# Performance work log

Hardware: AMD Instinct MI355X
Metric: run time of the kernel (lower is better)

Reference implementation:

```python
import jax, jax.numpy as jnp
import numpy as np

K = 512
D = 64


def setup_inputs() -> dict:
    key = jax.random.key(0)
    k1, k2 = jax.random.split(key)
    z_e_x = jax.random.normal(k1, (32, D, 64, 64), dtype=jnp.float32)  # [B, D, H, W]
    # codebook initialized uniform(-1/K, 1/K) as in the torch module
    emb = jax.random.uniform(k2, (K, D), dtype=jnp.float32, minval=-1.0 / K, maxval=1.0 / K)
    return {"z_e_x": z_e_x, "emb": emb}


def reference(z_e_x, emb):
    B, Dc, H, W = z_e_x.shape
    # [B, D, H, W] -> [B*H*W, D]
    z = jnp.transpose(z_e_x, (0, 2, 3, 1)).reshape(-1, Dc)
    z_norm = jnp.sum(z * z, axis=1, keepdims=True)          # [N, 1]
    e_norm = jnp.sum(emb * emb, axis=1)[None, :]            # [1, K]
    dists = z_norm + e_norm - 2.0 * (z @ emb.T)             # [N, K]
    dists = dists.reshape(B, H, W, -1)
    latents = jnp.argmin(dists, axis=-1)                    # [B, H, W] int
    return latents
```

## Files before the change

### kernel.cpp

```cpp
#include <hip/hip_runtime.h>

#define KCODES 512
#define DDIM   64
#define NROWS  131072

typedef short bf16x8 __attribute__((ext_vector_type(8)));
typedef float f32x4  __attribute__((ext_vector_type(4)));
typedef int   i32x4  __attribute__((ext_vector_type(4)));

union frag_cast { i32x4 i; bf16x8 h; };

__device__ __forceinline__ unsigned cvt_pk_bf16(float x0, float x1) {
    unsigned r;
    asm volatile("v_cvt_pk_bf16_f32 %0, %1, %2" : "=v"(r) : "v"(x0), "v"(x1));
    return r;
}

__device__ __forceinline__ void split_pair(float x0, float x1, unsigned& h, unsigned& l) {
    h = cvt_pk_bf16(x0, x1);
    float hf0 = __uint_as_float(h << 16);
    float hf1 = __uint_as_float(h & 0xffff0000u);
    l = cvt_pk_bf16(x0 - hf0, x1 - hf1);
}

__device__ __forceinline__ void gload16(const void* g, void* l) {
    __builtin_amdgcn_global_load_lds(
        (const __attribute__((address_space(1))) void*)g,
        (__attribute__((address_space(3))) void*)l, 16, 0, 0);
}

__global__ __launch_bounds__(64) void k1_prep(const float* __restrict__ emb,
                                              float* __restrict__ en, float* __restrict__ emaxp,
                                              i32x4* __restrict__ efP) {
    const int kt = blockIdx.x, t = threadIdx.x;
    const int krow = t & 15, gq = t >> 4;
    const int k = kt * 16 + krow;

    float er[16];
    float pz = 0.f;
#pragma unroll
    for (int c = 0; c < 2; ++c)
#pragma unroll
        for (int j = 0; j < 8; ++j) {
            float x = emb[k * DDIM + c * 32 + gq * 8 + j];
            er[c * 8 + j] = x;
            pz = fmaf(x, x, pz);
        }

#pragma unroll
    for (int c = 0; c < 2; ++c) {
        i32x4 wh, wl;
#pragma unroll
        for (int i = 0; i < 4; ++i) {
            unsigned h, l;
            split_pair(er[c * 8 + 2 * i], er[c * 8 + 2 * i + 1], h, l);
            wh[i] = (int)h;
            wl[i] = (int)l;
        }
        efP[kt * 256 + c * 64 + krow + 16 * gq]       = wh;
        efP[kt * 256 + (2 + c) * 64 + krow + 16 * gq] = wl;
    }

    pz += __shfl_xor(pz, 16);
    pz += __shfl_xor(pz, 32);
    if (t < 16) en[k] = pz;

    float m = pz;
#pragma unroll
    for (int sh = 1; sh <= 8; sh <<= 1) m = fmaxf(m, __shfl_xor(m, sh));
    if (t == 0) emaxp[kt] = m;
}

__global__ __launch_bounds__(256, 4) void k3_fused(
    const float* __restrict__ z, const float* __restrict__ emb,
    const i32x4* __restrict__ efP,
    const float* __restrict__ en_g, const float* __restrict__ emaxp,
    int* __restrict__ out) {

    __shared__ i32x4 sfrag[2][8][4][64];
    __shared__ float en_l[KCODES];
    __shared__ float zn_l[128];
    __shared__ float zrow_s[4][64];
    __shared__ int   flag_rows[128];
    __shared__ int   nflag;

    const int t = threadIdx.x, blk = blockIdx.x;
    const int n0 = blk * 128;
    const int b = n0 >> 12, hw0 = n0 & 4095;
    const int w = t >> 6, lane = t & 63;
    const int klane = lane & 15, g = lane >> 4;

    if (t == 0) nflag = 0;

    auto issue_chunk = [&](int kg, int bsel) {
        const i32x4* src = efP + (size_t)kg * 2048;
        i32x4* dst = &sfrag[bsel][0][0][0];
#pragma unroll
        for (int i = 0; i < 8; ++i) {
            int q = w * 8 + i;
            gload16(src + q * 64 + lane, dst + q * 64);
        }
    };
    issue_chunk(0, 0);

    en_l[t] = en_g[t];
    en_l[t + 256] = en_g[t + 256];

    float em2 = 0.f;
#pragma unroll
    for (int i = 0; i < 32; ++i) em2 = fmaxf(em2, emaxp[i]);
    const float emax = sqrtf(em2) * 1.0001f;

    const float* zbase = z + (size_t)b * (DDIM * 4096) + hw0;
    bf16x8 zh[2][2], zl[2][2];
#pragma unroll
    for (int tl = 0; tl < 2; ++tl) {
        const int row = w * 32 + tl * 16 + klane;
        float zv[16];
#pragma unroll
        for (int c = 0; c < 2; ++c)
#pragma unroll
            for (int j = 0; j < 8; ++j)
                zv[c * 8 + j] = zbase[(size_t)(c * 32 + g * 8 + j) * 4096 + row];
        float pz = 0.f;
#pragma unroll
        for (int c = 0; c < 2; ++c) {
            frag_cast uh, ul;
#pragma unroll
            for (int i = 0; i < 4; ++i) {
                float x0 = zv[c * 8 + 2 * i], x1 = zv[c * 8 + 2 * i + 1];
                pz = fmaf(x0, x0, pz);
                pz = fmaf(x1, x1, pz);
                unsigned h, l;
                split_pair(x0, x1, h, l);
                uh.i[i] = (int)h;
                ul.i[i] = (int)l;
            }
            zh[tl][c] = uh.h;
            zl[tl][c] = ul.h;
        }
        pz += __shfl_xor(pz, 16);
        pz += __shfl_xor(pz, 32);
        if (g == 0) zn_l[w * 32 + tl * 16 + klane] = pz;
    }

    float m1[2][4], m2[2][4];
    int i1[2][4];
#pragma unroll
    for (int tl = 0; tl < 2; ++tl)
#pragma unroll
        for (int r = 0; r < 4; ++r) { m1[tl][r] = 3.4e38f; m2[tl][r] = 3.4e38f; i1[tl][r] = 0; }

    f32x4 zero = {0.f, 0.f, 0.f, 0.f};

#pragma unroll 1
    for (int kg = 0; kg < 4; ++kg) {
        asm volatile("s_waitcnt vmcnt(0)" ::: "memory");
        __builtin_amdgcn_s_barrier();
        if (kg + 1 < 4) issue_chunk(kg + 1, (kg + 1) & 1);
        const int bsel = kg & 1;
#pragma unroll 2
        for (int ktl = 0; ktl < 8; ++ktl) {
            const int k = (kg * 8 + ktl) * 16 + klane;
            const float enk = en_l[k];
            frag_cast e0h, e1h, e0l, e1l;
            e0h.i = sfrag[bsel][ktl][0][lane];
            e1h.i = sfrag[bsel][ktl][1][lane];
            e0l.i = sfrag[bsel][ktl][2][lane];
            e1l.i = sfrag[bsel][ktl][3][lane];
#pragma unroll
            for (int tl = 0; tl < 2; ++tl) {
                f32x4 acc = __builtin_amdgcn_mfma_f32_16x16x32_bf16(zh[tl][0], e0h.h, zero, 0, 0, 0);
                acc = __builtin_amdgcn_mfma_f32_16x16x32_bf16(zh[tl][1], e1h.h, acc, 0, 0, 0);
                acc = __builtin_amdgcn_mfma_f32_16x16x32_bf16(zh[tl][0], e0l.h, acc, 0, 0, 0);
                acc = __builtin_amdgcn_mfma_f32_16x16x32_bf16(zh[tl][1], e1l.h, acc, 0, 0, 0);
                acc = __builtin_amdgcn_mfma_f32_16x16x32_bf16(zl[tl][0], e0h.h, acc, 0, 0, 0);
                acc = __builtin_amdgcn_mfma_f32_16x16x32_bf16(zl[tl][1], e1h.h, acc, 0, 0, 0);
#pragma unroll
                for (int r = 0; r < 4; ++r) {
                    float d = fmaf(-2.f, acc[r], enk);
                    float o1 = m1[tl][r];
                    i1[tl][r] = (d < o1) ? k : i1[tl][r];
                    m2[tl][r] = fminf(m2[tl][r], fmaxf(o1, d));
                    m1[tl][r] = fminf(o1, d);
                }
            }
        }
    }

#pragma unroll
    for (int sh = 1; sh <= 8; sh <<= 1) {
#pragma unroll
        for (int tl = 0; tl < 2; ++tl)
#pragma unroll
            for (int r = 0; r < 4; ++r) {
                float om1 = __shfl_xor(m1[tl][r], sh);
                int oi1 = __shfl_xor(i1[tl][r], sh);
                float om2 = __shfl_xor(m2[tl][r], sh);
                float hi = fmaxf(m1[tl][r], om1);
                m2[tl][r] = fminf(fminf(m2[tl][r], om2), hi);
                i1[tl][r] = (om1 < m1[tl][r]) ? oi1 : i1[tl][r];
                m1[tl][r] = fminf(m1[tl][r], om1);
            }
    }

    if (klane == 0) {
#pragma unroll
        for (int tl = 0; tl < 2; ++tl) {
            int rowbase = n0 + w * 32 + tl * 16 + g * 4;
            i32x4 idx4;
#pragma unroll
            for (int r = 0; r < 4; ++r) idx4[r] = i1[tl][r];
            *(i32x4*)(out + rowbase) = idx4;
#pragma unroll
            for (int r = 0; r < 4; ++r) {
                float zz = zn_l[w * 32 + tl * 16 + g * 4 + r];
                float W = fmaf(sqrtf(zz) * emax, 1.0e-4f, zz * 1.0e-6f);
                if (m2[tl][r] - m1[tl][r] <= W) {
                    int p = atomicAdd(&nflag, 1);
                    flag_rows[p] = w * 32 + tl * 16 + g * 4 + r;
                }
            }
        }
    }
    __syncthreads();

    const int nf = nflag;
    for (int i = w; i < nf; i += 4) {
        const int lrow = flag_rows[i];
        zrow_s[w][lane] = zbase[(size_t)lane * 4096 + lrow];
        const float znr = zn_l[lrow];
        float best = 3.4e38f;
        int bi = 0;
#pragma unroll 1
        for (int kk = 0; kk < 8; ++kk) {
            int k = lane * 8 + kk;
            const float* e0 = emb + k * DDIM;
            float acc = 0.f;
#pragma unroll
            for (int d = 0; d < DDIM; ++d) acc = fmaf(e0[d], zrow_s[w][d], acc);
            float dist = fmaf(-2.f, acc, znr + en_l[k]);
            if (dist < best) { best = dist; bi = k; }
        }
        unsigned long long key =
            ((unsigned long long)__float_as_uint(best) << 32) | (unsigned)bi;
#pragma unroll
        for (int sh = 32; sh; sh >>= 1) {
            unsigned long long o = __shfl_xor(key, sh);
            key = (o < key) ? o : key;
        }
        if (lane == 0) out[n0 + lrow] = (int)(key & 0xFFFFFFFFull);
    }
}

__global__ void fb_enorm(const float* __restrict__ emb, float* __restrict__ en) {
    int k = blockIdx.x * blockDim.x + threadIdx.x;
    if (k < KCODES) {
        float s = 0.f;
#pragma unroll
        for (int d = 0; d < DDIM; ++d) { float e = emb[k * DDIM + d]; s = fmaf(e, e, s); }
        en[k] = s;
    }
}
__global__ __launch_bounds__(256) void fb_argmin(const float* __restrict__ z,
                                                 const float* __restrict__ emb,
                                                 const float* __restrict__ en,
                                                 int* __restrict__ out, int nrows) {
    int n = blockIdx.x * blockDim.x + threadIdx.x;
    if (n >= nrows) return;
    int b = n >> 12, hw = n & 4095;
    const float* zp = z + (size_t)b * (DDIM * 4096) + hw;
    float zr[DDIM];
#pragma unroll
    for (int d = 0; d < DDIM; ++d) zr[d] = zp[(size_t)d * 4096];
    float zn = 0.f;
#pragma unroll
    for (int d = 0; d < DDIM; ++d) zn = fmaf(zr[d], zr[d], zn);
    float best = 3.4e38f; int bi = 0;
    for (int k0 = 0; k0 < KCODES; k0 += 8) {
        float acc[8];
#pragma unroll
        for (int kk = 0; kk < 8; ++kk) acc[kk] = 0.f;
        const float* e0 = emb + k0 * DDIM;
#pragma unroll
        for (int d = 0; d < DDIM; ++d) {
            float zd = zr[d];
#pragma unroll
            for (int kk = 0; kk < 8; ++kk) acc[kk] = fmaf(e0[kk * DDIM + d], zd, acc[kk]);
        }
#pragma unroll
        for (int kk = 0; kk < 8; ++kk) {
            float dist = fmaf(-2.f, acc[kk], zn + en[k0 + kk]);
            if (dist < best) { best = dist; bi = k0 + kk; }
        }
    }
    out[n] = bi;
}

extern "C" void kernel_launch(void* const* d_in, const int* in_sizes, int n_in,
                              void* d_out, int out_size, void* d_ws, size_t ws_size,
                              hipStream_t stream) {
    const float* z   = (const float*)d_in[0];
    const float* emb = (const float*)d_in[1];
    int* out = (int*)d_out;

    const size_t SZ_EF   = 32 * 4 * 64 * 16;
    const size_t SZ_EN   = KCODES * 4;
    const size_t SZ_EMAX = 128;
    const size_t NEED = SZ_EF + SZ_EN + SZ_EMAX;

    if (ws_size < NEED) {
        float* en = (float*)d_ws;
        fb_enorm<<<2, 256, 0, stream>>>(emb, en);
        fb_argmin<<<NROWS / 256, 256, 0, stream>>>(z, emb, en, out, NROWS);
        return;
    }

    char* p = (char*)d_ws;
    i32x4* efP = (i32x4*)p;   p += SZ_EF;
    float* en  = (float*)p;   p += SZ_EN;
    float* emaxp = (float*)p;

    k1_prep<<<32, 64, 0, stream>>>(emb, en, emaxp, efP);
    k3_fused<<<NROWS / 128, 256, 0, stream>>>(z, emb, efP, en, emaxp, out);
}
```

Baseline: 82.30 us.

## Halve rows per block and shrink codebook LDS chunks to raise occupancy

Each block now handles 64 rows, with one 16-row tile per wave, instead of 128. The codebook is streamed in 16 small double-buffered chunks of 8KB instead of 4 large 64KB ones, and the zrow scratch aliases the fragment buffer. Launch bounds rise to 8 blocks per CU to cut registers and LDS per block and improve latency hiding. In exchange, each codebook fragment is reused across half as many rows, and there are more barriers per block and twice as many blocks.

After: 103.7 us. 1.26x slower.

```diff
diff --git a/kernel.cpp b/kernel.cpp
--- a/kernel.cpp
+++ b/kernel.cpp
@@ -71,21 +71,22 @@
     if (t == 0) emaxp[kt] = m;
 }
 
-__global__ __launch_bounds__(256, 4) void k3_fused(
+__global__ __launch_bounds__(256, 8) void k3_fused(
     const float* __restrict__ z, const float* __restrict__ emb,
     const i32x4* __restrict__ efP,
     const float* __restrict__ en_g, const float* __restrict__ emaxp,
     int* __restrict__ out) {
 
-    __shared__ i32x4 sfrag[2][8][4][64];
+    __shared__ __align__(16) char smem_raw[16384];
     __shared__ float en_l[KCODES];
-    __shared__ float zn_l[128];
-    __shared__ float zrow_s[4][64];
-    __shared__ int   flag_rows[128];
+    __shared__ float zn_l[64];
+    __shared__ int   flag_rows[64];
     __shared__ int   nflag;
 
+    i32x4 (*sfrag)[2][4][64] = (i32x4(*)[2][4][64])smem_raw;
+
     const int t = threadIdx.x, blk = blockIdx.x;
-    const int n0 = blk * 128;
+    const int n0 = blk * 64;
     const int b = n0 >> 12, hw0 = n0 & 4095;
     const int w = t >> 6, lane = t & 63;
     const int klane = lane & 15, g = lane >> 4;
@@ -93,12 +94,13 @@
     if (t == 0) nflag = 0;
 
     auto issue_chunk = [&](int kg, int bsel) {
-        const i32x4* src = efP + (size_t)kg * 2048;
-        i32x4* dst = &sfrag[bsel][0][0][0];
-#pragma unroll
-        for (int i = 0; i < 8; ++i) {
-            int q = w * 8 + i;
-            gload16(src + q * 64 + lane, dst + q * 64);
+        const int kt0 = kg * 2;
+#pragma unroll
+        for (int i = 0; i < 2; ++i) {
+            int q = w * 2 + i;
+            int ktl = q >> 2, slot = q & 3;
+            gload16(efP + (size_t)(kt0 + ktl) * 256 + slot * 64 + lane,
+                    &sfrag[bsel][ktl][slot][0]);
         }
     };
     issue_chunk(0, 0);
@@ -112,10 +114,9 @@
     const float emax = sqrtf(em2) * 1.0001f;
 
     const float* zbase = z + (size_t)b * (DDIM * 4096) + hw0;
-    bf16x8 zh[2][2], zl[2][2];
-#pragma unroll
-    for (int tl = 0; tl < 2; ++tl) {
-        const int row = w * 32 + tl * 16 + klane;
+    const int row = w * 16 + klane;
+    bf16x8 zh[2], zl[2];
+    {
         float zv[16];
 #pragma unroll
         for (int c = 0; c < 2; ++c)
@@ -136,54 +137,50 @@
                 uh.i[i] = (int)h;
                 ul.i[i] = (int)l;
             }
-            zh[tl][c] = uh.h;
-            zl[tl][c] = ul.h;
+            zh[c] = uh.h;
+            zl[c] = ul.h;
         }
         pz += __shfl_xor(pz, 16);
         pz += __shfl_xor(pz, 32);
-        if (g == 0) zn_l[w * 32 + tl * 16 + klane] = pz;
-    }
-
-    float m1[2][4], m2[2][4];
-    int i1[2][4];
-#pragma unroll
-    for (int tl = 0; tl < 2; ++tl)
-#pragma unroll
-        for (int r = 0; r < 4; ++r) { m1[tl][r] = 3.4e38f; m2[tl][r] = 3.4e38f; i1[tl][r] = 0; }
+        if (g == 0) zn_l[w * 16 + klane] = pz;
+    }
+    __syncthreads();
+
+    float m1[4], m2[4];
+    int i1[4];
+#pragma unroll
+    for (int r = 0; r < 4; ++r) { m1[r] = 3.4e38f; m2[r] = 3.4e38f; i1[r] = 0; }
 
     f32x4 zero = {0.f, 0.f, 0.f, 0.f};
 
-#pragma unroll 1
-    for (int kg = 0; kg < 4; ++kg) {
+#pragma unroll 2
+    for (int kg = 0; kg < 16; ++kg) {
         asm volatile("s_waitcnt vmcnt(0)" ::: "memory");
         __builtin_amdgcn_s_barrier();
-        if (kg + 1 < 4) issue_chunk(kg + 1, (kg + 1) & 1);
+        if (kg + 1 < 16) issue_chunk(kg + 1, (kg + 1) & 1);
         const int bsel = kg & 1;
-#pragma unroll 2
-        for (int ktl = 0; ktl < 8; ++ktl) {
-            const int k = (kg * 8 + ktl) * 16 + klane;
+#pragma unroll
+        for (int ktl = 0; ktl < 2; ++ktl) {
+            const int k = (kg * 2 + ktl) * 16 + klane;
             const float enk = en_l[k];
             frag_cast e0h, e1h, e0l, e1l;
             e0h.i = sfrag[bsel][ktl][0][lane];
             e1h.i = sfrag[bsel][ktl][1][lane];
             e0l.i = sfrag[bsel][ktl][2][lane];
             e1l.i = sfrag[bsel][ktl][3][lane];
-#pragma unroll
-            for (int tl = 0; tl < 2; ++tl) {
-                f32x4 acc = __builtin_amdgcn_mfma_f32_16x16x32_bf16(zh[tl][0], e0h.h, zero, 0, 0, 0);
-                acc = __builtin_amdgcn_mfma_f32_16x16x32_bf16(zh[tl][1], e1h.h, acc, 0, 0, 0);
-                acc = __builtin_amdgcn_mfma_f32_16x16x32_bf16(zh[tl][0], e0l.h, acc, 0, 0, 0);
-                acc = __builtin_amdgcn_mfma_f32_16x16x32_bf16(zh[tl][1], e1l.h, acc, 0, 0, 0);
-                acc = __builtin_amdgcn_mfma_f32_16x16x32_bf16(zl[tl][0], e0h.h, acc, 0, 0, 0);
-                acc = __builtin_amdgcn_mfma_f32_16x16x32_bf16(zl[tl][1], e1h.h, acc, 0, 0, 0);
-#pragma unroll
-                for (int r = 0; r < 4; ++r) {
-                    float d = fmaf(-2.f, acc[r], enk);
-                    float o1 = m1[tl][r];
-                    i1[tl][r] = (d < o1) ? k : i1[tl][r];
-                    m2[tl][r] = fminf(m2[tl][r], fmaxf(o1, d));
-                    m1[tl][r] = fminf(o1, d);
-                }
+            f32x4 acc = __builtin_amdgcn_mfma_f32_16x16x32_bf16(zh[0], e0h.h, zero, 0, 0, 0);
+            acc = __builtin_amdgcn_mfma_f32_16x16x32_bf16(zl[0], e0h.h, acc, 0, 0, 0);
+            acc = __builtin_amdgcn_mfma_f32_16x16x32_bf16(zh[1], e1h.h, acc, 0, 0, 0);
+            acc = __builtin_amdgcn_mfma_f32_16x16x32_bf16(zl[1], e1h.h, acc, 0, 0, 0);
+            acc = __builtin_amdgcn_mfma_f32_16x16x32_bf16(zh[0], e0l.h, acc, 0, 0, 0);
+            acc = __builtin_amdgcn_mfma_f32_16x16x32_bf16(zh[1], e1l.h, acc, 0, 0, 0);
+#pragma unroll
+            for (int r = 0; r < 4; ++r) {
+                float d = fmaf(-2.f, acc[r], enk);
+                float o1 = m1[r];
+                i1[r] = (d < o1) ? k : i1[r];
+                m2[r] = fminf(m2[r], fmaxf(o1, d));
+                m1[r] = fminf(o1, d);
             }
         }
     }
@@ -191,40 +188,36 @@
 #pragma unroll
     for (int sh = 1; sh <= 8; sh <<= 1) {
 #pragma unroll
-        for (int tl = 0; tl < 2; ++tl)
-#pragma unroll
-            for (int r = 0; r < 4; ++r) {
-                float om1 = __shfl_xor(m1[tl][r], sh);
-                int oi1 = __shfl_xor(i1[tl][r], sh);
-                float om2 = __shfl_xor(m2[tl][r], sh);
-                float hi = fmaxf(m1[tl][r], om1);
-                m2[tl][r] = fminf(fminf(m2[tl][r], om2), hi);
-                i1[tl][r] = (om1 < m1[tl][r]) ? oi1 : i1[tl][r];
-                m1[tl][r] = fminf(m1[tl][r], om1);
+        for (int r = 0; r < 4; ++r) {
+            float om1 = __shfl_xor(m1[r], sh);
+            int oi1 = __shfl_xor(i1[r], sh);
+            float om2 = __shfl_xor(m2[r], sh);
+            float hi = fmaxf(m1[r], om1);
+            m2[r] = fminf(fminf(m2[r], om2), hi);
+            i1[r] = (om1 < m1[r]) ? oi1 : i1[r];
+            m1[r] = fminf(m1[r], om1);
+        }
+    }
+
+    if (klane == 0) {
+        int rowbase = n0 + w * 16 + g * 4;
+        i32x4 idx4;
+#pragma unroll
+        for (int r = 0; r < 4; ++r) idx4[r] = i1[r];
+        *(i32x4*)(out + rowbase) = idx4;
+#pragma unroll
+        for (int r = 0; r < 4; ++r) {
+            float zz = zn_l[w * 16 + g * 4 + r];
+            float W = fmaf(sqrtf(zz) * emax, 1.0e-4f, zz * 1.0e-6f);
+            if (m2[r] - m1[r] <= W) {
+                int p = atomicAdd(&nflag, 1);
+                flag_rows[p] = w * 16 + g * 4 + r;
             }
-    }
-
-    if (klane == 0) {
-#pragma unroll
-        for (int tl = 0; tl < 2; ++tl) {
-            int rowbase = n0 + w * 32 + tl * 16 + g * 4;
-            i32x4 idx4;
-#pragma unroll
-            for (int r = 0; r < 4; ++r) idx4[r] = i1[tl][r];
-            *(i32x4*)(out + rowbase) = idx4;
-#pragma unroll
-            for (int r = 0; r < 4; ++r) {
-                float zz = zn_l[w * 32 + tl * 16 + g * 4 + r];
-                float W = fmaf(sqrtf(zz) * emax, 1.0e-4f, zz * 1.0e-6f);
-                if (m2[tl][r] - m1[tl][r] <= W) {
-                    int p = atomicAdd(&nflag, 1);
-                    flag_rows[p] = w * 32 + tl * 16 + g * 4 + r;
-                }
-            }
         }
     }
     __syncthreads();
 
+    float (*zrow_s)[64] = (float(*)[64])smem_raw;
     const int nf = nflag;
     for (int i = w; i < nf; i += 4) {
         const int lrow = flag_rows[i];
@@ -322,5 +315,5 @@
     float* emaxp = (float*)p;
 
     k1_prep<<<32, 64, 0, stream>>>(emb, en, emaxp, efP);
-    k3_fused<<<NROWS / 128, 256, 0, stream>>>(z, emb, efP, en, emaxp, out);
-}
+    k3_fused<<<NROWS / 64, 256, 0, stream>>>(z, emb, efP, en, emaxp, out);
+}
```

## Use per-wave private double-buffered codebook staging and med3 second-min update

Applied to the files above, without the earlier changes.

Each wave now loads its own copy of each 16-code fragment tile into a private LDS double buffer, two tiles ahead, so the block-wide barriers between codebook chunks go away. The wait uses vmcnt(4) so the next tile's loads stay in flight. The second-minimum update is folded into a single v_med3_f32. The recheck scratch row now aliases the fragment buffer to keep LDS the same size. The cost is that every wave issues its own global loads, so L2/global traffic for codebook fragments is four times higher, and each tile's pipeline is shallower.

Measured after the change: 77.35 us, median of 2. 1.06x faster.

```diff
diff --git a/kernel.cpp b/kernel.cpp
--- a/kernel.cpp
+++ b/kernel.cpp
@@ -21,6 +21,12 @@
     float hf0 = __uint_as_float(h << 16);
     float hf1 = __uint_as_float(h & 0xffff0000u);
     l = cvt_pk_bf16(x0 - hf0, x1 - hf1);
+}
+
+__device__ __forceinline__ float med3(float a, float b, float c) {
+    float r;
+    asm volatile("v_med3_f32 %0, %1, %2, %3" : "=v"(r) : "v"(a), "v"(b), "v"(c));
+    return r;
 }
 
 __device__ __forceinline__ void gload16(const void* g, void* l) {
@@ -77,10 +83,9 @@
     const float* __restrict__ en_g, const float* __restrict__ emaxp,
     int* __restrict__ out) {
 
-    __shared__ i32x4 sfrag[2][8][4][64];
+    __shared__ i32x4 sfrag[4][2][4][64];
     __shared__ float en_l[KCODES];
     __shared__ float zn_l[128];
-    __shared__ float zrow_s[4][64];
     __shared__ int   flag_rows[128];
     __shared__ int   nflag;
 
@@ -91,17 +96,6 @@
     const int klane = lane & 15, g = lane >> 4;
 
     if (t == 0) nflag = 0;
-
-    auto issue_chunk = [&](int kg, int bsel) {
-        const i32x4* src = efP + (size_t)kg * 2048;
-        i32x4* dst = &sfrag[bsel][0][0][0];
-#pragma unroll
-        for (int i = 0; i < 8; ++i) {
-            int q = w * 8 + i;
-            gload16(src + q * 64 + lane, dst + q * 64);
-        }
-    };
-    issue_chunk(0, 0);
 
     en_l[t] = en_g[t];
     en_l[t + 256] = en_g[t + 256];
@@ -143,6 +137,7 @@
         pz += __shfl_xor(pz, 32);
         if (g == 0) zn_l[w * 32 + tl * 16 + klane] = pz;
     }
+    __syncthreads();
 
     float m1[2][4], m2[2][4];
     int i1[2][4];
@@ -153,37 +148,49 @@
 
     f32x4 zero = {0.f, 0.f, 0.f, 0.f};
 
+    auto issue = [&](int kt, int buf) {
+        const i32x4* src = efP + (size_t)kt * 256 + lane;
+        gload16(src,       &sfrag[w][buf][0][0]);
+        gload16(src + 64,  &sfrag[w][buf][1][0]);
+        gload16(src + 128, &sfrag[w][buf][2][0]);
+        gload16(src + 192, &sfrag[w][buf][3][0]);
+    };
+
+    issue(0, 0);
+    issue(1, 1);
+
 #pragma unroll 1
-    for (int kg = 0; kg < 4; ++kg) {
-        asm volatile("s_waitcnt vmcnt(0)" ::: "memory");
-        __builtin_amdgcn_s_barrier();
-        if (kg + 1 < 4) issue_chunk(kg + 1, (kg + 1) & 1);
-        const int bsel = kg & 1;
-#pragma unroll 2
-        for (int ktl = 0; ktl < 8; ++ktl) {
-            const int k = (kg * 8 + ktl) * 16 + klane;
-            const float enk = en_l[k];
-            frag_cast e0h, e1h, e0l, e1l;
-            e0h.i = sfrag[bsel][ktl][0][lane];
-            e1h.i = sfrag[bsel][ktl][1][lane];
-            e0l.i = sfrag[bsel][ktl][2][lane];
-            e1l.i = sfrag[bsel][ktl][3][lane];
-#pragma unroll
-            for (int tl = 0; tl < 2; ++tl) {
-                f32x4 acc = __builtin_amdgcn_mfma_f32_16x16x32_bf16(zh[tl][0], e0h.h, zero, 0, 0, 0);
-                acc = __builtin_amdgcn_mfma_f32_16x16x32_bf16(zh[tl][1], e1h.h, acc, 0, 0, 0);
-                acc = __builtin_amdgcn_mfma_f32_16x16x32_bf16(zh[tl][0], e0l.h, acc, 0, 0, 0);
-                acc = __builtin_amdgcn_mfma_f32_16x16x32_bf16(zh[tl][1], e1l.h, acc, 0, 0, 0);
-                acc = __builtin_amdgcn_mfma_f32_16x16x32_bf16(zl[tl][0], e0h.h, acc, 0, 0, 0);
-                acc = __builtin_amdgcn_mfma_f32_16x16x32_bf16(zl[tl][1], e1h.h, acc, 0, 0, 0);
-#pragma unroll
-                for (int r = 0; r < 4; ++r) {
-                    float d = fmaf(-2.f, acc[r], enk);
-                    float o1 = m1[tl][r];
-                    i1[tl][r] = (d < o1) ? k : i1[tl][r];
-                    m2[tl][r] = fminf(m2[tl][r], fmaxf(o1, d));
-                    m1[tl][r] = fminf(o1, d);
-                }
+    for (int kt = 0; kt < 32; ++kt) {
+        const int buf = kt & 1;
+        if (kt < 31) { asm volatile("s_waitcnt vmcnt(4)" ::: "memory"); }
+        else         { asm volatile("s_waitcnt vmcnt(0)" ::: "memory"); }
+
+        frag_cast e0h, e1h, e0l, e1l;
+        e0h.i = sfrag[w][buf][0][lane];
+        e1h.i = sfrag[w][buf][1][lane];
+        e0l.i = sfrag[w][buf][2][lane];
+        e1l.i = sfrag[w][buf][3][lane];
+        asm volatile("s_waitcnt lgkmcnt(0)" ::: "memory");
+        __builtin_amdgcn_sched_barrier(0);
+        if (kt < 30) issue(kt + 2, buf);
+
+        const int k = kt * 16 + klane;
+        const float enk = en_l[k];
+#pragma unroll
+        for (int tl = 0; tl < 2; ++tl) {
+            f32x4 acc = __builtin_amdgcn_mfma_f32_16x16x32_bf16(zh[tl][0], e0h.h, zero, 0, 0, 0);
+            acc = __builtin_amdgcn_mfma_f32_16x16x32_bf16(zh[tl][1], e1h.h, acc, 0, 0, 0);
+            acc = __builtin_amdgcn_mfma_f32_16x16x32_bf16(zh[tl][0], e0l.h, acc, 0, 0, 0);
+            acc = __builtin_amdgcn_mfma_f32_16x16x32_bf16(zh[tl][1], e1l.h, acc, 0, 0, 0);
+            acc = __builtin_amdgcn_mfma_f32_16x16x32_bf16(zl[tl][0], e0h.h, acc, 0, 0, 0);
+            acc = __builtin_amdgcn_mfma_f32_16x16x32_bf16(zl[tl][1], e1h.h, acc, 0, 0, 0);
+#pragma unroll
+            for (int r = 0; r < 4; ++r) {
+                float d = fmaf(-2.f, acc[r], enk);
+                float o1 = m1[tl][r];
+                i1[tl][r] = (d < o1) ? k : i1[tl][r];
+                m2[tl][r] = med3(o1, m2[tl][r], d);
+                m1[tl][r] = fminf(o1, d);
             }
         }
     }
@@ -225,6 +232,7 @@
     }
     __syncthreads();
 
+    float (*zrow_s)[64] = (float(*)[64])&sfrag[0][0][0][0];
     const int nf = nflag;
     for (int i = w; i < nf; i += 4) {
         const int lrow = flag_rows[i];
```
